# Kernel optimization log

Hardware: AMD Instinct MI355X
Metric: run time of the kernel (lower is better)

## Reference

```python
import jax, jax.numpy as jnp
import numpy as np

B, S, D = 2, 2048, 1024
H = 16
DK = D // H
FF = 4096
EPS = 1e-6


def setup_inputs() -> dict:
    key = jax.random.key(0)
    ks = jax.random.split(key, 16)
    sd = 0.02
    inp = {
        "x": jax.random.normal(ks[0], (B, S, D), dtype=jnp.float32),
        # attention projections (stored as [in, out]; y = x @ W + b)
        "Wq": jax.random.normal(ks[1], (D, D), dtype=jnp.float32) * sd,
        "bq": jnp.zeros((D,), jnp.float32),
        "Wk": jax.random.normal(ks[2], (D, D), dtype=jnp.float32) * sd,
        "bk": jnp.zeros((D,), jnp.float32),
        "Wv": jax.random.normal(ks[3], (D, D), dtype=jnp.float32) * sd,
        "bv": jnp.zeros((D,), jnp.float32),
        "Wo": jax.random.normal(ks[4], (D, D), dtype=jnp.float32) * sd,
        "bo": jnp.zeros((D,), jnp.float32),
        # FFN
        "W1": jax.random.normal(ks[5], (D, FF), dtype=jnp.float32) * sd,
        "b1": jnp.zeros((FF,), jnp.float32),
        "W2": jax.random.normal(ks[6], (FF, D), dtype=jnp.float32) * sd,
        "b2": jnp.zeros((D,), jnp.float32),
        # LayerNorms (pre-norm)
        "ln1_g": jnp.ones((D,), jnp.float32),
        "ln1_b": jnp.zeros((D,), jnp.float32),
        "ln2_g": jnp.ones((D,), jnp.float32),
        "ln2_b": jnp.zeros((D,), jnp.float32),
    }
    return inp


def _layer_norm(x, g, b):
    mu = jnp.mean(x, axis=-1, keepdims=True)
    var = jnp.mean(jnp.square(x - mu), axis=-1, keepdims=True)
    return (x - mu) * jax.lax.rsqrt(var + EPS) * g + b


def _attention(x, Wq, bq, Wk, bk, Wv, bv, Wo, bo):
    # project and split heads: [B,S,D] -> [B,H,S,DK]
    def split(t):
        return t.reshape(B, S, H, DK).transpose(0, 2, 1, 3)
    q = split(x @ Wq + bq)
    k = split(x @ Wk + bk)
    v = split(x @ Wv + bv)
    scores = jnp.einsum("bhqd,bhkd->bhqk", q, k) / jnp.sqrt(jnp.float32(DK))
    p = jax.nn.softmax(scores, axis=-1)  # no mask in forward path; dropout eval-mode
    o = jnp.einsum("bhqk,bhkd->bhqd", p, v)
    o = o.transpose(0, 2, 1, 3).reshape(B, S, D)
    return o @ Wo + bo


def reference(x, Wq, bq, Wk, bk, Wv, bv, Wo, bo, W1, b1, W2, b2,
              ln1_g, ln1_b, ln2_g, ln2_b):
    # sublayer 1: x + attn(LN(x))
    x = x + _attention(_layer_norm(x, ln1_g, ln1_b), Wq, bq, Wk, bk, Wv, bv, Wo, bo)
    # sublayer 2: x + FFN(LN(x))
    h = jax.nn.relu(_layer_norm(x, ln2_g, ln2_b) @ W1 + b1)
    x = x + (h @ W2 + b2)
    return x
```

## Files before the change

### kernel.cpp

```cpp
#include <hip/hip_runtime.h>


#define S_LEN 2048
#define DMODEL 1024
#define NHEADS 16
#define FFDIM 4096
#define MROWS 4096

typedef _Float16 f16;
typedef _Float16 f16x8 __attribute__((ext_vector_type(8)));
typedef __fp16 fp16x2 __attribute__((ext_vector_type(2)));
typedef float f32x4 __attribute__((ext_vector_type(4)));
typedef unsigned int u32;
typedef unsigned long long u64;
typedef unsigned long long u64x2 __attribute__((ext_vector_type(2)));

union Frag { f16x8 h; u64 q[2]; f16 e[8]; u32 w[4]; };

__device__ __forceinline__ f32x4 mfma16(f16x8 a, f16x8 b, f32x4 c) {
  return __builtin_amdgcn_mfma_f32_16x16x32_f16(a, b, c, 0, 0, 0);
}

__device__ __forceinline__ u32 pk16(float lo, float hi) {
  fp16x2 v = __builtin_amdgcn_cvt_pkrtz(lo, hi);
  return __builtin_bit_cast(u32, v);
}

typedef __attribute__((address_space(1))) const void gvoid;
typedef __attribute__((address_space(3))) void lvoid;

__device__ __forceinline__ void gload16(const f16* gp, f16* lp) {
  __builtin_amdgcn_global_load_lds((gvoid*)gp, (lvoid*)lp, 16, 0, 0);
}

__global__ __launch_bounds__(256) void wtrans_kernel(const float* __restrict__ W,
                                                     f16* __restrict__ Wt,
                                                     int K, int N) {
  __shared__ f16 tile[32][33];
  const int n0 = blockIdx.x * 32, k0 = blockIdx.y * 32;
  const int tx = threadIdx.x & 31, ty = threadIdx.x >> 5;
  for (int i = 0; i < 4; i++) {
    int k = ty + i * 8;
    tile[k][tx] = (f16)W[(size_t)(k0 + k) * N + n0 + tx];
  }
  __syncthreads();
  for (int i = 0; i < 4; i++) {
    int n = ty + i * 8;
    Wt[(size_t)(n0 + n) * K + k0 + tx] = tile[tx][n];
  }
}

__global__ __launch_bounds__(256) void wtrans4_kernel(const float* __restrict__ W0,
                                                      const float* __restrict__ W1,
                                                      const float* __restrict__ W2,
                                                      const float* __restrict__ W3,
                                                      f16* __restrict__ D0,
                                                      f16* __restrict__ D1,
                                                      f16* __restrict__ D2,
                                                      f16* __restrict__ D3) {
  const int z = blockIdx.z;
  const float* W = z == 0 ? W0 : z == 1 ? W1 : z == 2 ? W2 : W3;
  f16* Wt = z == 0 ? D0 : z == 1 ? D1 : z == 2 ? D2 : D3;
  __shared__ f16 tile[32][33];
  const int n0 = blockIdx.x * 32, k0 = blockIdx.y * 32;
  const int tx = threadIdx.x & 31, ty = threadIdx.x >> 5;
  for (int i = 0; i < 4; i++) {
    int k = ty + i * 8;
    tile[k][tx] = (f16)W[(size_t)(k0 + k) * 1024 + n0 + tx];
  }
  __syncthreads();
  for (int i = 0; i < 4; i++) {
    int n = ty + i * 8;
    Wt[(size_t)(n0 + n) * 1024 + k0 + tx] = tile[tx][n];
  }
}

__global__ void bias_concat_kernel(const float* __restrict__ bq,
                                   const float* __restrict__ bk,
                                   const float* __restrict__ bv,
                                   float* __restrict__ out) {
  int i = blockIdx.x * 256 + threadIdx.x;
  float v = (i < 1024) ? bq[i] : (i < 2048) ? bk[i - 1024] : bv[i - 2048];
  out[i] = v;
}

__global__ __launch_bounds__(256) void ln_kernel(const float* __restrict__ x,
                                                 const float* __restrict__ gw,
                                                 const float* __restrict__ bw,
                                                 f16* __restrict__ out) {
  const int row = blockIdx.x, t = threadIdx.x;
  const float* xr = x + (size_t)row * DMODEL;
  float4 v = *(const float4*)(xr + t * 4);
  float s = v.x + v.y + v.z + v.w;
  float s2 = v.x * v.x + v.y * v.y + v.z * v.z + v.w * v.w;
  for (int off = 1; off < 64; off <<= 1) {
    s += __shfl_xor(s, off);
    s2 += __shfl_xor(s2, off);
  }
  __shared__ float red[8];
  const int w = t >> 6, lane = t & 63;
  if (lane == 0) { red[w] = s; red[w + 4] = s2; }
  __syncthreads();
  s = red[0] + red[1] + red[2] + red[3];
  s2 = red[4] + red[5] + red[6] + red[7];
  float mu = s * (1.0f / DMODEL);
  float var = s2 * (1.0f / DMODEL) - mu * mu;
  float rstd = rsqrtf(var + 1e-6f);
  float4 g4 = *(const float4*)(gw + t * 4);
  float4 b4 = *(const float4*)(bw + t * 4);
  union { f16 h[4]; u64 q; } o;
  o.h[0] = (f16)((v.x - mu) * rstd * g4.x + b4.x);
  o.h[1] = (f16)((v.y - mu) * rstd * g4.y + b4.y);
  o.h[2] = (f16)((v.z - mu) * rstd * g4.z + b4.z);
  o.h[3] = (f16)((v.w - mu) * rstd * g4.w + b4.w);
  *(u64*)(out + (size_t)row * DMODEL + t * 4) = o.q;
}

template <int BM, int BN>
__global__ __launch_bounds__(256, 2) void gemm2(const f16* __restrict__ A, int lda,
                                                const f16* __restrict__ Bt, int ldb,
                                                const float* __restrict__ bias,
                                                const float* __restrict__ res,
                                                float* __restrict__ outf,
                                                f16* __restrict__ outh, int ldo,
                                                int N, int K, int relu) {
  constexpr int MT = BM / 32, NT = BN / 32;
  __shared__ f16 As[2][BM * 64];
  __shared__ f16 Bs[2][BN * 64];
  const int m0 = blockIdx.y * BM, n0 = blockIdx.x * BN;
  const int t = threadIdx.x;
  const int lane = t & 63, w = t >> 6;
  const int wr = w >> 1, wc = w & 1;
  const int rA = lane & 15, g = lane >> 4;

  f32x4 acc[MT][NT] = {};

  auto stageA = [&](int k0, int buf) {
#pragma unroll
    for (int p = 0; p < BM / 32; p++) {
      const int chunk = p * 256 + w * 64 + lane;
      const int row = chunk >> 3;
      const int cbg = ((chunk & 7) ^ (row & 7)) * 8;
      gload16(A + (size_t)(m0 + row) * lda + k0 + cbg,
              &As[buf][(p * 256 + w * 64) * 8]);
    }
  };
  auto stageB = [&](int k0, int buf) {
#pragma unroll
    for (int p = 0; p < BN / 32; p++) {
      const int chunk = p * 256 + w * 64 + lane;
      const int row = chunk >> 3;
      const int cbg = ((chunk & 7) ^ (row & 7)) * 8;
      gload16(Bt + (size_t)(n0 + row) * ldb + k0 + cbg,
              &Bs[buf][(p * 256 + w * 64) * 8]);
    }
  };

  auto compute = [&](int cur) {
#pragma unroll
    for (int ks = 0; ks < 2; ks++) {
      Frag a[MT], b[NT];
#pragma unroll
      for (int mt = 0; mt < MT; mt++) {
        const int row = wr * (BM / 2) + mt * 16 + rA;
        a[mt].h = *(const f16x8*)(&As[cur][row * 64 + ((ks * 4 + g) ^ (row & 7)) * 8]);
      }
#pragma unroll
      for (int nt = 0; nt < NT; nt++) {
        const int row = wc * (BN / 2) + nt * 16 + rA;
        b[nt].h = *(const f16x8*)(&Bs[cur][row * 64 + ((ks * 4 + g) ^ (row & 7)) * 8]);
      }
#pragma unroll
      for (int mt = 0; mt < MT; mt++)
#pragma unroll
        for (int nt = 0; nt < NT; nt++)
          acc[mt][nt] = mfma16(a[mt].h, b[nt].h, acc[mt][nt]);
    }
  };

  const int nsteps = K / 64;
  stageA(0, 0);
  stageB(0, 0);
  stageA(64, 1);

  for (int ts = 0; ts < nsteps - 1; ++ts) {
    const int cur = ts & 1;
    asm volatile("s_waitcnt vmcnt(4)" ::: "memory");
    __builtin_amdgcn_sched_barrier(0);
    __builtin_amdgcn_s_barrier();
    stageB(ts * 64 + 64, cur ^ 1);
    compute(cur);
    asm volatile("s_waitcnt lgkmcnt(0)" ::: "memory");
    __builtin_amdgcn_sched_barrier(0);
    __builtin_amdgcn_s_barrier();
    if (ts + 2 < nsteps) stageA(ts * 64 + 128, cur);
  }
  asm volatile("s_waitcnt vmcnt(0)" ::: "memory");
  __builtin_amdgcn_sched_barrier(0);
  __builtin_amdgcn_s_barrier();
  compute((nsteps - 1) & 1);

#pragma unroll
  for (int mt = 0; mt < MT; mt++) {
#pragma unroll
    for (int nt = 0; nt < NT; nt++) {
      const int col = n0 + wc * (BN / 2) + nt * 16 + rA;
      const int rowb = m0 + wr * (BM / 2) + mt * 16 + g * 4;
      const float bs = bias[col];
#pragma unroll
      for (int r = 0; r < 4; r++) {
        float v = acc[mt][nt][r] + bs;
        if (relu) v = fmaxf(v, 0.0f);
        if (res) v += res[(size_t)(rowb + r) * N + col];
        if (outf) outf[(size_t)(rowb + r) * N + col] = v;
        if (outh) outh[(size_t)(rowb + r) * ldo + col] = (f16)v;
      }
    }
  }
}

__global__ __launch_bounds__(256) void vtrans_kernel(const f16* __restrict__ qkv,
                                                     f16* __restrict__ vt) {
  const int bh = blockIdx.y;
  const int s0 = blockIdx.x * 64;
  const int b = bh >> 4, h = bh & 15;
  __shared__ f16 tile[64][72];
  const int t = threadIdx.x;
  for (int pass = 0; pass < 2; pass++) {
    int sl = (t >> 3) + pass * 32;
    int dk0 = (t & 7) * 8;
    u64x2 v = *(const u64x2*)(qkv + (size_t)(b * S_LEN + s0 + sl) * 3072 + 2048 + h * 64 + dk0);
    *(u64x2*)(&tile[sl][dk0]) = v;
  }
  __syncthreads();
  for (int pass = 0; pass < 2; pass++) {
    int dk = (t >> 3) + pass * 32;
    int sc = (t & 7) * 8;
    union { u64x2 q; f16 u[8]; } o;
    for (int j = 0; j < 8; j++) {
      int pos = sc + j;
      int kv = (pos & 32) | ((pos & 4) << 2) | ((pos & 0x18) >> 1) | (pos & 3);
      o.u[j] = tile[kv][dk];
    }
    *(u64x2*)(vt + (size_t)(bh * 64 + dk) * S_LEN + s0 + sc) = o.q;
  }
}

__global__ __launch_bounds__(256, 4) void attn_kernel(const f16* __restrict__ qkv,
                                                      const f16* __restrict__ vt,
                                                      f16* __restrict__ attn_out) {
  const int qt0 = blockIdx.x * 64;
  const int bh = blockIdx.y;
  const int b = bh >> 4, h = bh & 15;
  const int t = threadIdx.x;
  const int lane = t & 63, w = t >> 6;
  const int rA = lane & 15, g = lane >> 4;

  __shared__ f16 Ks[2][64 * 64];
  __shared__ f16 Vs[2][64 * 64];

  const int qrow = qt0 + w * 16 + rA;
  Frag qf[2];
#pragma unroll
  for (int kt = 0; kt < 2; kt++) {
    const f16* p = qkv + (size_t)(b * S_LEN + qrow) * 3072 + h * 64 + kt * 32 + 8 * g;
    f16x8 v = *(const f16x8*)p;
#pragma unroll
    for (int j = 0; j < 8; j++) v[j] = v[j] * (f16)0.18033688f;
    qf[kt].h = v;
  }

  float lR = 0.0f;
  f32x4 o2[4] = {};

#define STAGE_KV(kv0_, buf_)                                                     \
  {                                                                              \
    _Pragma("unroll") for (int i = 0; i < 2; i++) {                              \
      int C = i * 256 + w * 64 + lane;                                           \
      int row = C >> 3;                                                          \
      int cbg = ((C & 7) ^ (row & 7)) * 8;                                       \
      gload16(qkv + (size_t)(b * S_LEN + (kv0_) + row) * 3072 + 1024 + h * 64 + cbg, \
              &Ks[buf_][(i * 256 + w * 64) * 8]);                                \
      gload16(vt + (size_t)(bh * 64 + row) * S_LEN + (kv0_) + cbg,               \
              &Vs[buf_][(i * 256 + w * 64) * 8]);                                \
    }                                                                            \
  }

  int cur = 0;
  STAGE_KV(0, 0);

  for (int kv0 = 0; kv0 < S_LEN; kv0 += 64) {
    __syncthreads();
    if (kv0 + 64 < S_LEN) STAGE_KV(kv0 + 64, cur ^ 1);

    f32x4 s[4] = {};
#pragma unroll
    for (int nt = 0; nt < 4; nt++) {
      const int row = nt * 16 + rA;
#pragma unroll
      for (int kt = 0; kt < 2; kt++) {
        Frag kf;
        kf.h = *(const f16x8*)(&Ks[cur][row * 64 + ((kt * 4 + g) ^ (row & 7)) * 8]);
        s[nt] = mfma16(kf.h, qf[kt].h, s[nt]);
      }
    }

    float rs = 0.0f;
#pragma unroll
    for (int nt = 0; nt < 4; nt++)
#pragma unroll
      for (int r = 0; r < 4; r++) {
        float e0 = exp2f(s[nt][r]);
        s[nt][r] = e0;
        rs += e0;
      }
    rs += __shfl_xor(rs, 16);
    rs += __shfl_xor(rs, 32);
    lR += rs;

    Frag ph[2];
#pragma unroll
    for (int j = 0; j < 2; j++) {
      ph[j].w[0] = pk16(s[2 * j][0], s[2 * j][1]);
      ph[j].w[1] = pk16(s[2 * j][2], s[2 * j][3]);
      ph[j].w[2] = pk16(s[2 * j + 1][0], s[2 * j + 1][1]);
      ph[j].w[3] = pk16(s[2 * j + 1][2], s[2 * j + 1][3]);
    }

#pragma unroll
    for (int ntd = 0; ntd < 4; ntd++) {
      const int row = ntd * 16 + rA;
#pragma unroll
      for (int j = 0; j < 2; j++) {
        Frag vf;
        vf.h = *(const f16x8*)(&Vs[cur][row * 64 + ((j * 4 + g) ^ (row & 7)) * 8]);
        o2[ntd] = mfma16(vf.h, ph[j].h, o2[ntd]);
      }
    }

    cur ^= 1;
  }

  const float inv = 1.0f / lR;
#pragma unroll
  for (int ntd = 0; ntd < 4; ntd++) {
    union { f16 h[4]; u64 q; } pk;
#pragma unroll
    for (int r = 0; r < 4; r++) pk.h[r] = (f16)(o2[ntd][r] * inv);
    *(u64*)(attn_out + (size_t)(b * S_LEN + qrow) * DMODEL + h * 64 + ntd * 16 + g * 4) = pk.q;
  }
#undef STAGE_KV
}

extern "C" void kernel_launch(void* const* d_in, const int* in_sizes, int n_in,
                              void* d_out, int out_size, void* d_ws, size_t ws_size,
                              hipStream_t stream) {
  const float* x     = (const float*)d_in[0];
  const float* Wq    = (const float*)d_in[1];
  const float* bq    = (const float*)d_in[2];
  const float* Wk    = (const float*)d_in[3];
  const float* bk    = (const float*)d_in[4];
  const float* Wv    = (const float*)d_in[5];
  const float* bv    = (const float*)d_in[6];
  const float* Wo    = (const float*)d_in[7];
  const float* bo    = (const float*)d_in[8];
  const float* W1    = (const float*)d_in[9];
  const float* b1    = (const float*)d_in[10];
  const float* W2    = (const float*)d_in[11];
  const float* b2    = (const float*)d_in[12];
  const float* ln1g  = (const float*)d_in[13];
  const float* ln1b  = (const float*)d_in[14];
  const float* ln2g  = (const float*)d_in[15];
  const float* ln2b  = (const float*)d_in[16];
  float* out = (float*)d_out;
  char* ws = (char*)d_ws;

  size_t off = 0;
  f16* wqkv_t = (f16*)(ws + off); off += (size_t)3072 * 1024 * 2;
  f16* wo_t   = (f16*)(ws + off); off += (size_t)1024 * 1024 * 2;
  f16* w1_t   = (f16*)(ws + off); off += (size_t)4096 * 1024 * 2;
  f16* w2_t   = (f16*)(ws + off); off += (size_t)1024 * 4096 * 2;
  float* bqkv = (float*)(ws + off); off += 3072 * 4;
  f16* regB   = (f16*)(ws + off); off += (size_t)MROWS * 1024 * 2;
  f16* qkv    = (f16*)(ws + off); off += (size_t)MROWS * 3072 * 2;
  f16* vt     = (f16*)(ws + off); off += (size_t)MROWS * 1024 * 2;
  f16* hbuf   = qkv;

  wtrans4_kernel<<<dim3(32, 32, 4), 256, 0, stream>>>(
      Wq, Wk, Wv, Wo,
      wqkv_t, wqkv_t + (size_t)1024 * 1024, wqkv_t + (size_t)2048 * 1024, wo_t);
  wtrans_kernel<<<dim3(128, 32), 256, 0, stream>>>(W1, w1_t, 1024, 4096);
  wtrans_kernel<<<dim3(32, 128), 256, 0, stream>>>(W2, w2_t, 4096, 1024);
  bias_concat_kernel<<<12, 256, 0, stream>>>(bq, bk, bv, bqkv);

  ln_kernel<<<MROWS, 256, 0, stream>>>(x, ln1g, ln1b, regB);

  gemm2<128, 128><<<dim3(24, 32), 256, 0, stream>>>(regB, 1024, wqkv_t, 1024, bqkv,
                                                    nullptr, nullptr, qkv, 3072,
                                                    3072, 1024, 0);
  vtrans_kernel<<<dim3(32, 32), 256, 0, stream>>>(qkv, vt);

  attn_kernel<<<dim3(32, 32), 256, 0, stream>>>(qkv, vt, regB);

  gemm2<128, 64><<<dim3(16, 32), 256, 0, stream>>>(regB, 1024, wo_t, 1024, bo,
                                                   x, out, nullptr, 0,
                                                   1024, 1024, 0);
  ln_kernel<<<MROWS, 256, 0, stream>>>(out, ln2g, ln2b, regB);

  gemm2<128, 128><<<dim3(32, 32), 256, 0, stream>>>(regB, 1024, w1_t, 1024, b1,
                                                    nullptr, nullptr, hbuf, 4096,
                                                    4096, 1024, 1);
  gemm2<128, 64><<<dim3(16, 32), 256, 0, stream>>>(hbuf, 4096, w2_t, 4096, b2,
                                                   out, out, nullptr, 0,
                                                   1024, 4096, 0);
}
```

Before: 280.4 us.

## Switch GEMM to 32x32x16 MFMA and remap workgroup ids for XCD locality

Replaces the 16x16x32 MFMA tiles in the generic GEMM with 32x32x16 MFMA instructions. This cuts LDS fragment loads per MFMA and raises arithmetic intensity per register fragment, and the epilogue and LDS read indexing are rewritten to match the new accumulator layout. It also permutes the block id so consecutive tiles land on the same XCD, which should improve L2 reuse. Risks include higher register pressure from the 16-wide accumulators, and the remap assumes the block count divides by 8.

```diff
diff --git a/kernel.cpp b/kernel.cpp
--- a/kernel.cpp
+++ b/kernel.cpp
@@ -11,6 +11,7 @@
 typedef _Float16 f16x8 __attribute__((ext_vector_type(8)));
 typedef __fp16 fp16x2 __attribute__((ext_vector_type(2)));
 typedef float f32x4 __attribute__((ext_vector_type(4)));
+typedef float f32x16 __attribute__((ext_vector_type(16)));
 typedef unsigned int u32;
 typedef unsigned long long u64;
 typedef unsigned long long u64x2 __attribute__((ext_vector_type(2)));
@@ -19,6 +20,9 @@
 
 __device__ __forceinline__ f32x4 mfma16(f16x8 a, f16x8 b, f32x4 c) {
   return __builtin_amdgcn_mfma_f32_16x16x32_f16(a, b, c, 0, 0, 0);
+}
+__device__ __forceinline__ f32x16 mfma32(f16x8 a, f16x8 b, f32x16 c) {
+  return __builtin_amdgcn_mfma_f32_32x32x16_f16(a, b, c, 0, 0, 0);
 }
 
 __device__ __forceinline__ u32 pk16(float lo, float hi) {
@@ -124,16 +128,20 @@
                                                 float* __restrict__ outf,
                                                 f16* __restrict__ outh, int ldo,
                                                 int N, int K, int relu) {
-  constexpr int MT = BM / 32, NT = BN / 32;
+  constexpr int MT2 = BM / 64, NT2 = BN / 64;
   __shared__ f16 As[2][BM * 64];
   __shared__ f16 Bs[2][BN * 64];
-  const int m0 = blockIdx.y * BM, n0 = blockIdx.x * BN;
+  const int gx = gridDim.x;
+  const int nwg = gx * gridDim.y;
+  int id = blockIdx.y * gx + blockIdx.x;
+  id = (id & 7) * (nwg >> 3) + (id >> 3);
+  const int m0 = (id / gx) * BM, n0 = (id % gx) * BN;
   const int t = threadIdx.x;
   const int lane = t & 63, w = t >> 6;
   const int wr = w >> 1, wc = w & 1;
-  const int rA = lane & 15, g = lane >> 4;
-
-  f32x4 acc[MT][NT] = {};
+  const int l31 = lane & 31, lh = lane >> 5;
+
+  f32x16 acc[MT2][NT2] = {};
 
   auto stageA = [&](int k0, int buf) {
 #pragma unroll
@@ -158,23 +166,25 @@
 
   auto compute = [&](int cur) {
 #pragma unroll
-    for (int ks = 0; ks < 2; ks++) {
-      Frag a[MT], b[NT];
-#pragma unroll
-      for (int mt = 0; mt < MT; mt++) {
-        const int row = wr * (BM / 2) + mt * 16 + rA;
-        a[mt].h = *(const f16x8*)(&As[cur][row * 64 + ((ks * 4 + g) ^ (row & 7)) * 8]);
-      }
-#pragma unroll
-      for (int nt = 0; nt < NT; nt++) {
-        const int row = wc * (BN / 2) + nt * 16 + rA;
-        b[nt].h = *(const f16x8*)(&Bs[cur][row * 64 + ((ks * 4 + g) ^ (row & 7)) * 8]);
-      }
-#pragma unroll
-      for (int mt = 0; mt < MT; mt++)
-#pragma unroll
-        for (int nt = 0; nt < NT; nt++)
-          acc[mt][nt] = mfma16(a[mt].h, b[nt].h, acc[mt][nt]);
+    for (int ks = 0; ks < 4; ks++) {
+      Frag a[MT2], b[NT2];
+#pragma unroll
+      for (int mt = 0; mt < MT2; mt++) {
+        const int row = wr * (BM / 2) + mt * 32 + l31;
+        const int cb = (ks * 2 + lh) ^ (row & 7);
+        a[mt].h = *(const f16x8*)(&As[cur][row * 64 + cb * 8]);
+      }
+#pragma unroll
+      for (int nt = 0; nt < NT2; nt++) {
+        const int row = wc * (BN / 2) + nt * 32 + l31;
+        const int cb = (ks * 2 + lh) ^ (row & 7);
+        b[nt].h = *(const f16x8*)(&Bs[cur][row * 64 + cb * 8]);
+      }
+#pragma unroll
+      for (int mt = 0; mt < MT2; mt++)
+#pragma unroll
+        for (int nt = 0; nt < NT2; nt++)
+          acc[mt][nt] = mfma32(a[mt].h, b[nt].h, acc[mt][nt]);
     }
   };
 
@@ -201,19 +211,20 @@
   compute((nsteps - 1) & 1);
 
 #pragma unroll
-  for (int mt = 0; mt < MT; mt++) {
-#pragma unroll
-    for (int nt = 0; nt < NT; nt++) {
-      const int col = n0 + wc * (BN / 2) + nt * 16 + rA;
-      const int rowb = m0 + wr * (BM / 2) + mt * 16 + g * 4;
+  for (int mt = 0; mt < MT2; mt++) {
+#pragma unroll
+    for (int nt = 0; nt < NT2; nt++) {
+      const int col = n0 + wc * (BN / 2) + nt * 32 + l31;
+      const int rb = m0 + wr * (BM / 2) + mt * 32 + 4 * lh;
       const float bs = bias[col];
 #pragma unroll
-      for (int r = 0; r < 4; r++) {
-        float v = acc[mt][nt][r] + bs;
+      for (int reg = 0; reg < 16; reg++) {
+        const int row = rb + (reg & 3) + 8 * (reg >> 2);
+        float v = acc[mt][nt][reg] + bs;
         if (relu) v = fmaxf(v, 0.0f);
-        if (res) v += res[(size_t)(rowb + r) * N + col];
-        if (outf) outf[(size_t)(rowb + r) * N + col] = v;
-        if (outh) outh[(size_t)(rowb + r) * ldo + col] = (f16)v;
+        if (res) v += res[(size_t)row * N + col];
+        if (outf) outf[(size_t)row * N + col] = v;
+        if (outh) outh[(size_t)row * ldo + col] = (f16)v;
       }
     }
   }
```

Result: slower. 302.6 us (+7.9%).
